# Optimization experiments

Hardware: AMD Instinct MI355X
Metric: run time of the kernel (lower is better)

Reference implementation:

```python
import jax, jax.numpy as jnp
import numpy as np

NHEAD = 8

def layernorm(x, g, b, eps=1e-5):
    mu = x.mean(-1, keepdims=True)
    var = ((x - mu) ** 2).mean(-1, keepdims=True)
    return (x - mu) / jnp.sqrt(var + eps) * g + b

def linear_attention(q, k, v, eps=1e-6):
    # LoFTR kernelized linear attention: phi(x) = elu(x) + 1
    Q = jax.nn.elu(q) + 1.0          # [n, l, h, d]
    K = jax.nn.elu(k) + 1.0          # [n, s, h, d]
    s_len = v.shape[1]
    KV = jnp.einsum("nshd,nshv->nhdv", K, v / s_len)
    Z = 1.0 / (jnp.einsum("nlhd,nhd->nlh", Q, K.sum(axis=1)) + eps)
    return jnp.einsum("nlhd,nhdv,nlh->nlhv", Q, KV, Z) * s_len

def _block(x_base, q, k, v, Wm, W1, W2, g1, b1, g2, b2):
    bs, L, h, dh = q.shape
    msg = linear_attention(q, k, v).reshape(bs, L, h * dh)
    msg = layernorm(msg @ Wm, g1, b1)
    hcat = jnp.concatenate([x_base, msg], axis=2)          # [bs, L, 2*d]
    out = jax.nn.relu(hcat @ W1) @ W2
    return layernorm(out, g2, b2)

def setup_inputs() -> dict:
    key = jax.random.key(0)
    ks = jax.random.split(key, 8)
    bs, L, S, d = 8, 4800, 4800, 256
    w = lambda k, i, o: jax.random.normal(k, (i, o), jnp.float32) * 0.02
    return {
        "x": jax.random.normal(ks[0], (bs, L, d), jnp.float32),
        "source": jax.random.normal(ks[1], (bs, S, d), jnp.float32),
        "Wq": w(ks[2], d, d), "Wk": w(ks[3], d, d), "Wv": w(ks[4], d, d),
        "Wm": w(ks[5], d, d),
        "W1": w(ks[6], 2 * d, 2 * d), "W2": w(ks[7], 2 * d, d),
        "g1": jnp.ones((d,), jnp.float32), "b1": jnp.zeros((d,), jnp.float32),
        "g2": jnp.ones((d,), jnp.float32), "b2": jnp.zeros((d,), jnp.float32),
    }

def reference(x, source, Wq, Wk, Wv, Wm, W1, W2, g1, b1, g2, b2):
    bs, L, d = x.shape
    h = NHEAD
    dh = d // h
    q = (x @ Wq).reshape(bs, L, h, dh)
    k = (source @ Wk).reshape(bs, -1, h, dh)
    v = (source @ Wv).reshape(bs, -1, h, dh)
    # permute-then-view reinterpretations, exactly as in the torch code
    p13 = lambda t: t.transpose(0, 1, 3, 2).reshape(bs, -1, h, dh)  # permute(0,1,3,2)
    p21 = lambda t: t.transpose(0, 2, 1, 3).reshape(bs, -1, h, dh)  # permute(0,2,1,3)
    p32 = lambda t: t.transpose(0, 3, 2, 1).reshape(bs, -1, h, dh)  # permute(0,3,2,1)
    blk = lambda xb, qq, kk, vv: _block(xb, qq, kk, vv, Wm, W1, W2, g1, b1, g2, b2)
    m = blk(x, q, k, v)
    m3 = blk(x, p13(q), p13(k), p13(v))
    x_mid = x + 0.5 * (m + m3)
    m1 = blk(x_mid, p21(q), p21(k), p21(v))
    m2 = blk(x_mid, p32(q), p32(k), p32(v))
    return x_mid + 0.5 * (m1 + m2)
```

## Files before the change

kernel.cpp:

```cpp
#include <hip/hip_runtime.h>
#include <type_traits>
#include <cstdint>
#include <cstddef>

#define L_SEQ 4800
#define DMODEL 256
#define BS 8
#define MROWS (BS*L_SEQ)
#define PERBATCH (L_SEQ*DMODEL)
#define KVSET 67584

typedef __attribute__((ext_vector_type(8))) short bfrag8;
typedef __attribute__((ext_vector_type(4))) float floatx4;

__device__ __forceinline__ float bf2f(unsigned short u){
  union { unsigned int i; float f; } x; x.i = ((unsigned int)u) << 16; return x.f;
}
__device__ __forceinline__ unsigned short f2bf(float f){
  union { float f; unsigned int i; } x; x.f = f;
  x.i += 0x7fff + ((x.i >> 16) & 1);
  return (unsigned short)(x.i >> 16);
}
__device__ __forceinline__ float phi(float x){
  return x > 0.f ? x + 1.f : __expf(x);
}

template<typename TC, bool RELU>
__global__ __launch_bounds__(256) void gemm_mfma(const unsigned short* __restrict__ A,
                                                 const unsigned short* __restrict__ Bt,
                                                 TC* __restrict__ C, int M, int N, int K){
  __shared__ unsigned short Al[128*32];
  __shared__ unsigned short Bl[128*32];
  const int tid  = threadIdx.x;
  const int lane = tid & 63;
  const int wave = tid >> 6;
  const int row0 = blockIdx.y << 7;
  const int col0 = blockIdx.x << 7;
  const int wr0  = (wave & 1) << 6;
  const int wc0  = (wave >> 1) << 6;

  floatx4 acc[4][4] = {};

  const int i0 = tid, i1 = tid + 256;
  const int r0 = i0 >> 2, s0 = i0 & 3;
  const int r1 = i1 >> 2, s1 = i1 & 3;
  const int m = lane & 15, q = lane >> 4;

  for (int k0 = 0; k0 < K; k0 += 32){
    const unsigned short* ga0 = A  + (size_t)(row0 + r0)*K + k0 + s0*8;
    const unsigned short* ga1 = A  + (size_t)(row0 + r1)*K + k0 + s1*8;
    const unsigned short* gb0 = Bt + (size_t)(col0 + r0)*K + k0 + s0*8;
    const unsigned short* gb1 = Bt + (size_t)(col0 + r1)*K + k0 + s1*8;
    __builtin_amdgcn_global_load_lds((const __attribute__((address_space(1))) unsigned int*)ga0,
        (__attribute__((address_space(3))) unsigned int*)(Al + (size_t)i0*8), 16, 0, 0);
    __builtin_amdgcn_global_load_lds((const __attribute__((address_space(1))) unsigned int*)ga1,
        (__attribute__((address_space(3))) unsigned int*)(Al + (size_t)i1*8), 16, 0, 0);
    __builtin_amdgcn_global_load_lds((const __attribute__((address_space(1))) unsigned int*)gb0,
        (__attribute__((address_space(3))) unsigned int*)(Bl + (size_t)i0*8), 16, 0, 0);
    __builtin_amdgcn_global_load_lds((const __attribute__((address_space(1))) unsigned int*)gb1,
        (__attribute__((address_space(3))) unsigned int*)(Bl + (size_t)i1*8), 16, 0, 0);
    __builtin_amdgcn_s_waitcnt(0);
    __syncthreads();

    bfrag8 af[4], bf[4];
    #pragma unroll
    for (int t = 0; t < 4; t++){
      af[t] = *(const bfrag8*)(Al + (size_t)(wr0 + t*16 + m)*32 + q*8);
      bf[t] = *(const bfrag8*)(Bl + (size_t)(wc0 + t*16 + m)*32 + q*8);
    }
    #pragma unroll
    for (int mt = 0; mt < 4; mt++)
      #pragma unroll
      for (int nt = 0; nt < 4; nt++)
        acc[mt][nt] = __builtin_amdgcn_mfma_f32_16x16x32_bf16(af[mt], bf[nt], acc[mt][nt], 0, 0, 0);
    __syncthreads();
  }

  #pragma unroll
  for (int mt = 0; mt < 4; mt++){
    #pragma unroll
    for (int nt = 0; nt < 4; nt++){
      const int col  = col0 + wc0 + nt*16 + m;
      const int rowb = row0 + wr0 + mt*16 + q*4;
      #pragma unroll
      for (int i = 0; i < 4; i++){
        float v = acc[mt][nt][i];
        if (RELU) v = v > 0.f ? v : 0.f;
        if constexpr (std::is_same<TC,float>::value) C[(size_t)(rowb+i)*N + col] = v;
        else                                         C[(size_t)(rowb+i)*N + col] = f2bf(v);
      }
    }
  }
}

__global__ __launch_bounds__(256) void wconv(const float* __restrict__ W, unsigned short* __restrict__ Wt,
                                             int kshift, int N){
  int idx = blockIdx.x*256 + threadIdx.x;
  int kk = idx & ((1 << kshift) - 1);
  int nn = idx >> kshift;
  Wt[idx] = f2bf(W[(size_t)kk*N + nn]);
}
__global__ __launch_bounds__(256) void conv_bf16(const float* __restrict__ in, unsigned short* __restrict__ out){
  int i = blockIdx.x*256 + threadIdx.x;
  float4 v = ((const float4*)in)[i];
  ushort4 o; o.x = f2bf(v.x); o.y = f2bf(v.y); o.z = f2bf(v.z); o.w = f2bf(v.w);
  ((ushort4*)out)[i] = o;
}

__global__ __launch_bounds__(256) void permute1(const unsigned short* __restrict__ sA, unsigned short* __restrict__ dA,
                                                const unsigned short* __restrict__ sB, unsigned short* __restrict__ dB){
  const unsigned short* s = blockIdx.z ? sB : sA;
  unsigned short*       d = blockIdx.z ? dB : dA;
  __shared__ unsigned short tile[1024];
  const int t = threadIdx.x;
  const size_t base = (size_t)blockIdx.x * 1024;
  #pragma unroll
  for (int i = 0; i < 4; i++) tile[i*256 + t] = s[base + i*256 + t];
  __syncthreads();
  const int pg = ((t & 7) << 5) + (t >> 3);
  #pragma unroll
  for (int i = 0; i < 4; i++) d[base + i*256 + t] = tile[i*256 + pg];
}

__global__ __launch_bounds__(256) void permute2(const unsigned short* __restrict__ sA, unsigned short* __restrict__ dA,
                                                const unsigned short* __restrict__ sB, unsigned short* __restrict__ dB){
  const unsigned short* s = blockIdx.z ? sB : sA;
  unsigned short*       d = blockIdx.z ? dB : dA;
  __shared__ unsigned short tile[64*256];
  const int t = threadIdx.x;
  const int rr0 = blockIdx.x * 64;
  const size_t boff = (size_t)blockIdx.y * PERBATCH;
  #pragma unroll
  for (int i = 0; i < 16; i++){
    int u = i*256 + t;
    *(ushort4*)&tile[u*4] = *(const ushort4*)&s[boff + (size_t)rr0*256 + (size_t)u*4];
  }
  __syncthreads();
  #pragma unroll
  for (int i = 0; i < 8; i++){
    #pragma unroll
    for (int w = 0; w < 2; w++){
      int u = w*256 + t;
      int rr = u >> 3, c4 = (u & 7) << 2;
      ushort4 v = *(const ushort4*)&tile[rr*256 + i*32 + c4];
      *(ushort4*)&d[boff + (size_t)i*153600 + (size_t)rr0*32 + (size_t)u*4] = v;
    }
  }
}

__global__ __launch_bounds__(256) void permute3(const unsigned short* __restrict__ sA, unsigned short* __restrict__ dA,
                                                const unsigned short* __restrict__ sB, unsigned short* __restrict__ dB){
  const unsigned short* s = blockIdx.z ? sB : sA;
  unsigned short*       d = blockIdx.z ? dB : dA;
  __shared__ unsigned short tile[64*258];
  const int t = threadIdx.x;
  const int ll0 = blockIdx.x * 64;
  const size_t boff = (size_t)blockIdx.y * PERBATCH;
  #pragma unroll
  for (int i = 0; i < 32; i++){
    int u = i*256 + t;
    int row = u >> 7, col = (u & 127) << 1;
    *(ushort2*)&tile[row*258 + col] = *(const ushort2*)&s[boff + (size_t)(ll0+row)*256 + col];
  }
  __syncthreads();
  const int cw = t >> 6;
  const int ll = t & 63;
  #pragma unroll
  for (int cc = 0; cc < 256; cc += 4){
    int c = cc + cw;
    int sigma = ((c & 31) << 3) + (c >> 5);
    d[boff + (size_t)sigma*4800 + ll0 + ll] = tile[ll*258 + c];
  }
}

__global__ __launch_bounds__(256) void attn_stats(const unsigned short* __restrict__ kq,
                                                  const unsigned short* __restrict__ vq,
                                                  float* __restrict__ KV, float* __restrict__ Ksum){
  const int chunk = blockIdx.x, h = blockIdx.y, n = blockIdx.z;
  const int t = threadIdx.x;
  const int d = t >> 3;
  const int w4 = (t & 7) << 2;
  const size_t boff = (size_t)n * PERBATCH;
  __shared__ float kb[8][32], vb[8][32];
  const int lr = t >> 5, lj = t & 31;
  float a0=0.f, a1=0.f, a2=0.f, a3=0.f, ks=0.f;
  const int s0 = chunk * 240;
  for (int s = s0; s < s0 + 240; s += 8){
    int srci = (s + lr)*256 + (h << 5) + lj;
    kb[lr][lj] = phi(bf2f(kq[boff + srci]));
    vb[lr][lj] = bf2f(vq[boff + srci]);
    __syncthreads();
    #pragma unroll
    for (int r = 0; r < 8; r++){
      float kd = kb[r][d];
      ks += kd;
      a0 += kd * vb[r][w4+0];
      a1 += kd * vb[r][w4+1];
      a2 += kd * vb[r][w4+2];
      a3 += kd * vb[r][w4+3];
    }
    __syncthreads();
  }
  float* kvp = KV + (size_t)((((n<<3)+h)<<5) + d)*32 + w4;
  atomicAdd(kvp+0, a0);
  atomicAdd(kvp+1, a1);
  atomicAdd(kvp+2, a2);
  atomicAdd(kvp+3, a3);
  if ((t & 7) == 0) atomicAdd(Ksum + (((n<<3)+h)<<5) + d, ks);
}

__global__ __launch_bounds__(256) void attn_apply(const unsigned short* __restrict__ qq,
                                                  const float* __restrict__ KV,
                                                  const float* __restrict__ Ksum,
                                                  unsigned short* __restrict__ msg){
  __shared__ float kvs[8192];
  __shared__ float kss[256];
  __shared__ float Qs[4096];
  const int t = threadIdx.x;
  const int n = blockIdx.y;
  const int row0 = blockIdx.x << 4;
  const size_t boff = (size_t)n * PERBATCH;

  #pragma unroll
  for (int i = 0; i < 32; i++) kvs[i*256 + t] = KV[(size_t)n*8192 + i*256 + t];
  kss[t] = Ksum[n*256 + t];
  #pragma unroll
  for (int r = 0; r < 16; r++)
    Qs[r*256 + t] = phi(bf2f(qq[boff + (size_t)(row0 + r)*256 + t]));
  __syncthreads();

  const int h = t >> 5, w = t & 31;
  const float* kvh = kvs + h*1024;
  const float* ksh = kss + h*32;
  float acc[16], den[16];
  #pragma unroll
  for (int r = 0; r < 16; r++){ acc[r] = 0.f; den[r] = 1e-6f; }

  #pragma unroll
  for (int d4 = 0; d4 < 8; d4++){
    const float k0 = kvh[(d4*4+0)*32 + w];
    const float k1 = kvh[(d4*4+1)*32 + w];
    const float k2 = kvh[(d4*4+2)*32 + w];
    const float k3 = kvh[(d4*4+3)*32 + w];
    const float s0 = ksh[d4*4+0], s1 = ksh[d4*4+1], s2 = ksh[d4*4+2], s3 = ksh[d4*4+3];
    #pragma unroll
    for (int r = 0; r < 16; r++){
      float4 qv = *(const float4*)&Qs[r*256 + h*32 + d4*4];
      acc[r] += qv.x*k0 + qv.y*k1 + qv.z*k2 + qv.w*k3;
      den[r] += qv.x*s0 + qv.y*s1 + qv.z*s2 + qv.w*s3;
    }
  }
  #pragma unroll
  for (int r = 0; r < 16; r++)
    msg[boff + (size_t)(row0 + r)*256 + t] = f2bf(acc[r]/den[r]);
}

__device__ __forceinline__ float waveSum(float v){
  #pragma unroll
  for (int o = 32; o > 0; o >>= 1) v += __shfl_xor(v, o, 64);
  return v;
}

__global__ __launch_bounds__(256) void ln_bf16(const float* __restrict__ X, const float* __restrict__ g,
                                               const float* __restrict__ b, unsigned short* __restrict__ dst,
                                               int stride, int off){
  const int lane = threadIdx.x & 63;
  const int row = blockIdx.x*4 + (threadIdx.x >> 6);
  float4 v = ((const float4*)(X + (size_t)row*256))[lane];
  float mu = waveSum(v.x + v.y + v.z + v.w) * (1.f/256.f);
  float x0 = v.x - mu, x1 = v.y - mu, x2 = v.z - mu, x3 = v.w - mu;
  float var = waveSum(x0*x0 + x1*x1 + x2*x2 + x3*x3) * (1.f/256.f);
  float rs = rsqrtf(var + 1e-5f);
  float4 gv = ((const float4*)g)[lane];
  float4 bv = ((const float4*)b)[lane];
  ushort4 o;
  o.x = f2bf(x0*rs*gv.x + bv.x);
  o.y = f2bf(x1*rs*gv.y + bv.y);
  o.z = f2bf(x2*rs*gv.z + bv.z);
  o.w = f2bf(x3*rs*gv.w + bv.w);
  ((ushort4*)(dst + (size_t)row*stride + off))[lane] = o;
}

__global__ __launch_bounds__(256) void ln_acc(const float* __restrict__ X, const float* __restrict__ g,
                                              const float* __restrict__ b, float* __restrict__ macc, int add){
  const int lane = threadIdx.x & 63;
  const int row = blockIdx.x*4 + (threadIdx.x >> 6);
  float4 v = ((const float4*)(X + (size_t)row*256))[lane];
  float mu = waveSum(v.x + v.y + v.z + v.w) * (1.f/256.f);
  float x0 = v.x - mu, x1 = v.y - mu, x2 = v.z - mu, x3 = v.w - mu;
  float var = waveSum(x0*x0 + x1*x1 + x2*x2 + x3*x3) * (1.f/256.f);
  float rs = rsqrtf(var + 1e-5f);
  float4 gv = ((const float4*)g)[lane];
  float4 bv = ((const float4*)b)[lane];
  float4 y;
  y.x = x0*rs*gv.x + bv.x;
  y.y = x1*rs*gv.y + bv.y;
  y.z = x2*rs*gv.z + bv.z;
  y.w = x3*rs*gv.w + bv.w;
  float4* mp = (float4*)(macc + (size_t)row*256) + lane;
  if (add){
    float4 old = *mp;
    y.x += old.x; y.y += old.y; y.z += old.z; y.w += old.w;
  }
  *mp = y;
}

__global__ __launch_bounds__(256) void fill_hcat(const float* __restrict__ x, unsigned short* __restrict__ hcat){
  size_t i = (size_t)blockIdx.x*256 + threadIdx.x;
  hcat[(i >> 8)*512 + (i & 255)] = f2bf(x[i]);
}
__global__ __launch_bounds__(256) void xmid_k(const float* __restrict__ x, const float* __restrict__ macc,
                                              float* __restrict__ xmid, unsigned short* __restrict__ hcat){
  size_t i = (size_t)blockIdx.x*256 + threadIdx.x;
  float v = x[i] + 0.5f*macc[i];
  xmid[i] = v;
  hcat[(i >> 8)*512 + (i & 255)] = f2bf(v);
}
__global__ __launch_bounds__(256) void final_k(float* __restrict__ out, const float* __restrict__ macc){
  size_t i = (size_t)blockIdx.x*256 + threadIdx.x;
  out[i] = out[i] + 0.5f*macc[i];
}
__global__ __launch_bounds__(256) void zero_k(float* __restrict__ p, int n){
  int i = blockIdx.x*256 + threadIdx.x;
  if (i < n) p[i] = 0.f;
}

extern "C" void kernel_launch(void* const* d_in, const int* in_sizes, int n_in,
                              void* d_out, int out_size, void* d_ws, size_t ws_size,
                              hipStream_t stream){
  const float* x   = (const float*)d_in[0];
  const float* src = (const float*)d_in[1];
  const float* Wq  = (const float*)d_in[2];
  const float* Wk  = (const float*)d_in[3];
  const float* Wv  = (const float*)d_in[4];
  const float* Wm  = (const float*)d_in[5];
  const float* W1  = (const float*)d_in[6];
  const float* W2  = (const float*)d_in[7];
  const float* g1  = (const float*)d_in[8];
  const float* b1  = (const float*)d_in[9];
  const float* g2  = (const float*)d_in[10];
  const float* b2  = (const float*)d_in[11];
  float* out = (float*)d_out;

  char* ws = (char*)d_ws;
  size_t off = 0;
  auto alloc = [&](size_t bytes) -> void* {
    void* p = ws + off;
    off += (bytes + 255) & ~(size_t)255;
    return p;
  };
  unsigned short* qB    = (unsigned short*)alloc((size_t)MROWS*256*2);
  unsigned short* kB    = (unsigned short*)alloc((size_t)MROWS*256*2);
  unsigned short* vB    = (unsigned short*)alloc((size_t)MROWS*256*2);
  unsigned short* hcatB = (unsigned short*)alloc((size_t)MROWS*512*2);
  float* t1   = (float*)alloc((size_t)MROWS*256*4);
  float* macc = (float*)alloc((size_t)MROWS*256*4);
  float* KV4  = (float*)alloc((size_t)4*KVSET*4);
  unsigned short* WqT = (unsigned short*)alloc((size_t)256*256*2);
  unsigned short* WkT = (unsigned short*)alloc((size_t)256*256*2);
  unsigned short* WvT = (unsigned short*)alloc((size_t)256*256*2);
  unsigned short* WmT = (unsigned short*)alloc((size_t)256*256*2);
  unsigned short* W1T = (unsigned short*)alloc((size_t)512*512*2);
  unsigned short* W2T = (unsigned short*)alloc((size_t)256*512*2);
  (void)ws_size; (void)in_sizes; (void)n_in; (void)out_size;

  unsigned short* msgB  = kB;
  unsigned short* hidB  = kB;
  unsigned short* srcbf = (unsigned short*)t1;
  unsigned short* xbf   = srcbf + (size_t)MROWS*256;
  unsigned short* qP    = (unsigned short*)t1;
  unsigned short* kP    = (unsigned short*)macc;
  unsigned short* vP    = kP + (size_t)MROWS*256;
  float* xmid = out;

  const dim3 blk(256);

  wconv<<<dim3(256),  blk, 0, stream>>>(Wq, WqT, 8, 256);
  wconv<<<dim3(256),  blk, 0, stream>>>(Wk, WkT, 8, 256);
  wconv<<<dim3(256),  blk, 0, stream>>>(Wv, WvT, 8, 256);
  wconv<<<dim3(256),  blk, 0, stream>>>(Wm, WmT, 8, 256);
  wconv<<<dim3(1024), blk, 0, stream>>>(W1, W1T, 9, 512);
  wconv<<<dim3(512),  blk, 0, stream>>>(W2, W2T, 9, 256);
  conv_bf16<<<dim3(9600), blk, 0, stream>>>(src, srcbf);
  conv_bf16<<<dim3(9600), blk, 0, stream>>>(x,   xbf);

  gemm_mfma<unsigned short, false><<<dim3(2,300), blk, 0, stream>>>(xbf,   WqT, qB, MROWS, 256, 256);
  gemm_mfma<unsigned short, false><<<dim3(2,300), blk, 0, stream>>>(srcbf, WkT, kB, MROWS, 256, 256);
  gemm_mfma<unsigned short, false><<<dim3(2,300), blk, 0, stream>>>(srcbf, WvT, vB, MROWS, 256, 256);

  zero_k<<<dim3(1056), blk, 0, stream>>>(KV4, 4*KVSET);
  attn_stats<<<dim3(20,8,8), blk, 0, stream>>>(kB, vB, KV4 + 0*KVSET, KV4 + 0*KVSET + 65536);
  permute1<<<dim3(9600,1,2), blk, 0, stream>>>(kB, kP, vB, vP);
  attn_stats<<<dim3(20,8,8), blk, 0, stream>>>(kP, vP, KV4 + 1*KVSET, KV4 + 1*KVSET + 65536);
  permute2<<<dim3(75,8,2),  blk, 0, stream>>>(kB, kP, vB, vP);
  attn_stats<<<dim3(20,8,8), blk, 0, stream>>>(kP, vP, KV4 + 2*KVSET, KV4 + 2*KVSET + 65536);
  permute3<<<dim3(75,8,2),  blk, 0, stream>>>(kB, kP, vB, vP);
  attn_stats<<<dim3(20,8,8), blk, 0, stream>>>(kP, vP, KV4 + 3*KVSET, KV4 + 3*KVSET + 65536);

  fill_hcat<<<dim3(MROWS), blk, 0, stream>>>(x, hcatB);

  auto run_block = [&](int mode, int add){
    const float* KV   = KV4 + (size_t)mode*KVSET;
    const float* Ksum = KV + 65536;
    const unsigned short* qsrc = qB;
    if (mode == 1){ permute1<<<dim3(9600,1,1), blk, 0, stream>>>(qB, qP, nullptr, nullptr); qsrc = qP; }
    else if (mode == 2){ permute2<<<dim3(75,8,1), blk, 0, stream>>>(qB, qP, nullptr, nullptr); qsrc = qP; }
    else if (mode == 3){ permute3<<<dim3(75,8,1), blk, 0, stream>>>(qB, qP, nullptr, nullptr); qsrc = qP; }
    attn_apply<<<dim3(300,BS), blk, 0, stream>>>(qsrc, KV, Ksum, msgB);
    gemm_mfma<float, false><<<dim3(2,300), blk, 0, stream>>>(msgB, WmT, t1, MROWS, 256, 256);
    ln_bf16<<<dim3(9600), blk, 0, stream>>>(t1, g1, b1, hcatB, 512, 256);
    gemm_mfma<unsigned short, true><<<dim3(4,300), blk, 0, stream>>>(hcatB, W1T, hidB, MROWS, 512, 512);
    gemm_mfma<float, false><<<dim3(2,300), blk, 0, stream>>>(hidB, W2T, t1, MROWS, 256, 512);
    ln_acc<<<dim3(9600), blk, 0, stream>>>(t1, g2, b2, macc, add);
  };

  run_block(0, 0);
  run_block(1, 1);
  xmid_k<<<dim3(MROWS), blk, 0, stream>>>(x, macc, xmid, hcatB);
  run_block(2, 0);
  run_block(3, 1);
  final_k<<<dim3(MROWS), blk, 0, stream>>>(out, macc);
}
```

Baseline: 998.8 us.

## Fuse attention apply with Wm GEMM+LN, and FFN GEMMs with final LN

Replaces the six-kernel per-block chain (attn_apply, Wm GEMM, LN, W1 GEMM, W2 GEMM, LN-accumulate) with two fused kernels. attn_fused computes the linear-attention message for 64 rows into swizzled LDS, multiplies by Wm with MFMA, applies layernorm and writes bf16 into hcat. ffn_fused keeps the ReLU hidden tile in LDS between the W1 and W2 GEMMs using double-buffered global-to-LDS staging, then applies layernorm and accumulates into macc. This removes the fp32 intermediate round trips through global memory and several launches, at the cost of heavy LDS use (about 138KB per block in the FFN) and lower occupancy.

```diff
diff --git a/kernel.cpp b/kernel.cpp
--- a/kernel.cpp
+++ b/kernel.cpp
@@ -23,6 +23,10 @@
 }
 __device__ __forceinline__ float phi(float x){
   return x > 0.f ? x + 1.f : __expf(x);
+}
+__device__ __forceinline__ void gll16(const void* g, void* l){
+  __builtin_amdgcn_global_load_lds((const __attribute__((address_space(1))) unsigned int*)g,
+      (__attribute__((address_space(3))) unsigned int*)l, 16, 0, 0);
 }
 
 template<typename TC, bool RELU>
@@ -51,14 +55,10 @@
     const unsigned short* ga1 = A  + (size_t)(row0 + r1)*K + k0 + s1*8;
     const unsigned short* gb0 = Bt + (size_t)(col0 + r0)*K + k0 + s0*8;
     const unsigned short* gb1 = Bt + (size_t)(col0 + r1)*K + k0 + s1*8;
-    __builtin_amdgcn_global_load_lds((const __attribute__((address_space(1))) unsigned int*)ga0,
-        (__attribute__((address_space(3))) unsigned int*)(Al + (size_t)i0*8), 16, 0, 0);
-    __builtin_amdgcn_global_load_lds((const __attribute__((address_space(1))) unsigned int*)ga1,
-        (__attribute__((address_space(3))) unsigned int*)(Al + (size_t)i1*8), 16, 0, 0);
-    __builtin_amdgcn_global_load_lds((const __attribute__((address_space(1))) unsigned int*)gb0,
-        (__attribute__((address_space(3))) unsigned int*)(Bl + (size_t)i0*8), 16, 0, 0);
-    __builtin_amdgcn_global_load_lds((const __attribute__((address_space(1))) unsigned int*)gb1,
-        (__attribute__((address_space(3))) unsigned int*)(Bl + (size_t)i1*8), 16, 0, 0);
+    gll16(ga0, Al + (size_t)i0*8);
+    gll16(ga1, Al + (size_t)i1*8);
+    gll16(gb0, Bl + (size_t)i0*8);
+    gll16(gb1, Bl + (size_t)i1*8);
     __builtin_amdgcn_s_waitcnt(0);
     __syncthreads();
 
@@ -209,100 +209,291 @@
   if ((t & 7) == 0) atomicAdd(Ksum + (((n<<3)+h)<<5) + d, ks);
 }
 
-__global__ __launch_bounds__(256) void attn_apply(const unsigned short* __restrict__ qq,
+__global__ __launch_bounds__(256) void attn_fused(const unsigned short* __restrict__ qq,
                                                   const float* __restrict__ KV,
                                                   const float* __restrict__ Ksum,
-                                                  unsigned short* __restrict__ msg){
+                                                  const unsigned short* __restrict__ WmT,
+                                                  const float* __restrict__ g1,
+                                                  const float* __restrict__ b1,
+                                                  unsigned short* __restrict__ hcat){
   __shared__ float kvs[8192];
-  __shared__ float kss[256];
-  __shared__ float Qs[4096];
+  __shared__ char  msgL[32768];
+  __shared__ char  pool[16384];
   const int t = threadIdx.x;
   const int n = blockIdx.y;
-  const int row0 = blockIdx.x << 4;
+  const int row0 = blockIdx.x << 6;
   const size_t boff = (size_t)n * PERBATCH;
 
   #pragma unroll
   for (int i = 0; i < 32; i++) kvs[i*256 + t] = KV[(size_t)n*8192 + i*256 + t];
-  kss[t] = Ksum[n*256 + t];
-  #pragma unroll
-  for (int r = 0; r < 16; r++)
-    Qs[r*256 + t] = phi(bf2f(qq[boff + (size_t)(row0 + r)*256 + t]));
-  __syncthreads();
+  const float kssv = Ksum[n*256 + t];
 
   const int h = t >> 5, w = t & 31;
   const float* kvh = kvs + h*1024;
-  const float* ksh = kss + h*32;
-  float acc[16], den[16];
-  #pragma unroll
-  for (int r = 0; r < 16; r++){ acc[r] = 0.f; den[r] = 1e-6f; }
-
-  #pragma unroll
-  for (int d4 = 0; d4 < 8; d4++){
-    const float k0 = kvh[(d4*4+0)*32 + w];
-    const float k1 = kvh[(d4*4+1)*32 + w];
-    const float k2 = kvh[(d4*4+2)*32 + w];
-    const float k3 = kvh[(d4*4+3)*32 + w];
-    const float s0 = ksh[d4*4+0], s1 = ksh[d4*4+1], s2 = ksh[d4*4+2], s3 = ksh[d4*4+3];
-    #pragma unroll
-    for (int r = 0; r < 16; r++){
-      float4 qv = *(const float4*)&Qs[r*256 + h*32 + d4*4];
-      acc[r] += qv.x*k0 + qv.y*k1 + qv.z*k2 + qv.w*k3;
-      den[r] += qv.x*s0 + qv.y*s1 + qv.z*s2 + qv.w*s3;
-    }
-  }
-  #pragma unroll
-  for (int r = 0; r < 16; r++)
-    msg[boff + (size_t)(row0 + r)*256 + t] = f2bf(acc[r]/den[r]);
-}
-
-__device__ __forceinline__ float waveSum(float v){
-  #pragma unroll
-  for (int o = 32; o > 0; o >>= 1) v += __shfl_xor(v, o, 64);
-  return v;
-}
-
-__global__ __launch_bounds__(256) void ln_bf16(const float* __restrict__ X, const float* __restrict__ g,
-                                               const float* __restrict__ b, unsigned short* __restrict__ dst,
-                                               int stride, int off){
-  const int lane = threadIdx.x & 63;
-  const int row = blockIdx.x*4 + (threadIdx.x >> 6);
-  float4 v = ((const float4*)(X + (size_t)row*256))[lane];
-  float mu = waveSum(v.x + v.y + v.z + v.w) * (1.f/256.f);
-  float x0 = v.x - mu, x1 = v.y - mu, x2 = v.z - mu, x3 = v.w - mu;
-  float var = waveSum(x0*x0 + x1*x1 + x2*x2 + x3*x3) * (1.f/256.f);
-  float rs = rsqrtf(var + 1e-5f);
-  float4 gv = ((const float4*)g)[lane];
-  float4 bv = ((const float4*)b)[lane];
-  ushort4 o;
-  o.x = f2bf(x0*rs*gv.x + bv.x);
-  o.y = f2bf(x1*rs*gv.y + bv.y);
-  o.z = f2bf(x2*rs*gv.z + bv.z);
-  o.w = f2bf(x3*rs*gv.w + bv.w);
-  ((ushort4*)(dst + (size_t)row*stride + off))[lane] = o;
-}
-
-__global__ __launch_bounds__(256) void ln_acc(const float* __restrict__ X, const float* __restrict__ g,
-                                              const float* __restrict__ b, float* __restrict__ macc, int add){
-  const int lane = threadIdx.x & 63;
-  const int row = blockIdx.x*4 + (threadIdx.x >> 6);
-  float4 v = ((const float4*)(X + (size_t)row*256))[lane];
-  float mu = waveSum(v.x + v.y + v.z + v.w) * (1.f/256.f);
-  float x0 = v.x - mu, x1 = v.y - mu, x2 = v.z - mu, x3 = v.w - mu;
-  float var = waveSum(x0*x0 + x1*x1 + x2*x2 + x3*x3) * (1.f/256.f);
-  float rs = rsqrtf(var + 1e-5f);
-  float4 gv = ((const float4*)g)[lane];
-  float4 bv = ((const float4*)b)[lane];
-  float4 y;
-  y.x = x0*rs*gv.x + bv.x;
-  y.y = x1*rs*gv.y + bv.y;
-  y.z = x2*rs*gv.z + bv.z;
-  y.w = x3*rs*gv.w + bv.w;
-  float4* mp = (float4*)(macc + (size_t)row*256) + lane;
-  if (add){
-    float4 old = *mp;
-    y.x += old.x; y.y += old.y; y.z += old.z; y.w += old.w;
-  }
-  *mp = y;
+  float* Qs = (float*)pool;
+
+  for (int p = 0; p < 8; p++){
+    #pragma unroll
+    for (int r = 0; r < 8; r++)
+      Qs[r*256 + t] = phi(bf2f(qq[boff + (size_t)(row0 + p*8 + r)*256 + t]));
+    __syncthreads();
+
+    float acc[8], den[8];
+    #pragma unroll
+    for (int r = 0; r < 8; r++){
+      float dd = Qs[r*256 + t] * kssv;
+      #pragma unroll
+      for (int o = 1; o < 32; o <<= 1) dd += __shfl_xor(dd, o, 64);
+      den[r] = dd + 1e-6f;
+      acc[r] = 0.f;
+    }
+    #pragma unroll
+    for (int d4 = 0; d4 < 8; d4++){
+      const float k0v = kvh[(d4*4+0)*32 + w];
+      const float k1v = kvh[(d4*4+1)*32 + w];
+      const float k2v = kvh[(d4*4+2)*32 + w];
+      const float k3v = kvh[(d4*4+3)*32 + w];
+      #pragma unroll
+      for (int r = 0; r < 8; r++){
+        float4 qv = *(const float4*)&Qs[r*256 + h*32 + d4*4];
+        acc[r] += qv.x*k0v + qv.y*k1v + qv.z*k2v + qv.w*k3v;
+      }
+    }
+    #pragma unroll
+    for (int r = 0; r < 8; r++){
+      int lrow = p*8 + r;
+      int byte = (lrow << 9) + (t << 1);
+      byte ^= (lrow & 7) << 4;
+      *(unsigned short*)(msgL + byte) = f2bf(acc[r] / den[r]);
+    }
+    __syncthreads();
+  }
+
+  const int wave = t >> 6, lane = t & 63, m = lane & 15, qd = lane >> 4;
+  float gv[16], bv[16];
+  #pragma unroll
+  for (int nt = 0; nt < 16; nt++){ gv[nt] = g1[nt*16 + m]; bv[nt] = b1[nt*16 + m]; }
+
+  floatx4 acc[16] = {};
+  for (int ks = 0; ks < 8; ks++){
+    const int k0 = ks << 5;
+    #pragma unroll
+    for (int i = 0; i < 4; i++){
+      int u = (i << 8) + t;
+      int c = u >> 2, q4 = u & 3;
+      gll16(WmT + (size_t)c*256 + k0 + ((q4 ^ (c & 3)) << 3), pool + (u << 4));
+    }
+    asm volatile("s_waitcnt vmcnt(0)" ::: "memory");
+    __builtin_amdgcn_s_barrier();
+    asm volatile("" ::: "memory");
+    const int arow = (wave << 4) + m;
+    int abyte = (arow << 9) + (ks << 6) + (qd << 4);
+    abyte ^= (m & 7) << 4;
+    bfrag8 af = *(const bfrag8*)(msgL + abyte);
+    #pragma unroll
+    for (int nt = 0; nt < 16; nt++){
+      int col = (nt << 4) + m;
+      bfrag8 bf = *(const bfrag8*)(pool + col*64 + ((qd ^ (m & 3)) << 4));
+      acc[nt] = __builtin_amdgcn_mfma_f32_16x16x32_bf16(af, bf, acc[nt], 0, 0, 0);
+    }
+    asm volatile("" ::: "memory");
+    __builtin_amdgcn_s_barrier();
+    asm volatile("" ::: "memory");
+  }
+
+  float mu[4], rs[4];
+  #pragma unroll
+  for (int i = 0; i < 4; i++){
+    float s = 0.f, q = 0.f;
+    #pragma unroll
+    for (int nt = 0; nt < 16; nt++){ float v = acc[nt][i]; s += v; q += v*v; }
+    #pragma unroll
+    for (int o = 1; o < 16; o <<= 1){ s += __shfl_xor(s, o, 64); q += __shfl_xor(q, o, 64); }
+    float mean = s * (1.f/256.f);
+    float var  = q * (1.f/256.f) - mean*mean;
+    mu[i] = mean; rs[i] = rsqrtf(var + 1e-5f);
+  }
+  #pragma unroll
+  for (int nt = 0; nt < 16; nt++){
+    #pragma unroll
+    for (int i = 0; i < 4; i++){
+      int row = (wave << 4) + (qd << 2) + i;
+      int col = (nt << 4) + m;
+      int byte = (row << 9) + (col << 1);
+      byte ^= (row & 7) << 4;
+      *(unsigned short*)(msgL + byte) = f2bf((acc[nt][i] - mu[i]) * rs[i] * gv[nt] + bv[nt]);
+    }
+  }
+  __syncthreads();
+  const size_t gbase = (size_t)(n*4800 + row0) * 512;
+  #pragma unroll
+  for (int i = 0; i < 16; i++){
+    int u = (i << 8) + t;
+    int row = u >> 6, j = u & 63;
+    int byte = ((row << 9) + (j << 3)) ^ ((row & 7) << 4);
+    *(ushort4*)(hcat + gbase + (size_t)row*512 + 256 + (j << 2)) = *(const ushort4*)(msgL + byte);
+  }
+}
+
+__global__ __launch_bounds__(512) void ffn_fused(const unsigned short* __restrict__ hcat,
+                                                 const unsigned short* __restrict__ W1T,
+                                                 const unsigned short* __restrict__ W2T,
+                                                 const float* __restrict__ g2,
+                                                 const float* __restrict__ b2,
+                                                 float* __restrict__ macc, int add){
+  __shared__ char stg[73728];
+  __shared__ char hidm[65536];
+  const int tid = threadIdx.x;
+  const int wave = tid >> 6, lane = tid & 63;
+  const int rg = wave >> 1, ch = wave & 1;
+  const int m = lane & 15, qd = lane >> 4;
+  const int row0 = blockIdx.x << 6;
+
+  float gv[8], bv[8];
+  #pragma unroll
+  for (int nt = 0; nt < 8; nt++){
+    int col = (ch << 7) + nt*16 + m;
+    gv[nt] = g2[col]; bv[nt] = b2[col];
+  }
+
+  auto stage1 = [&](int ks, int b){
+    const int k0 = ks << 5;
+    {
+      int u = tid & 255;
+      int r = u >> 2, q4 = u & 3;
+      gll16(hcat + (size_t)(row0 + r)*512 + k0 + ((q4 ^ (r & 3)) << 3),
+            stg + (b << 12) + (u << 4));
+    }
+    #pragma unroll
+    for (int i = 0; i < 4; i++){
+      int u = (i << 9) + tid;
+      int c = u >> 2, q4 = u & 3;
+      gll16(W1T + (size_t)c*512 + k0 + ((q4 ^ (c & 3)) << 3),
+            stg + 8192 + (b << 15) + (u << 4));
+    }
+  };
+
+  floatx4 acc1[16] = {};
+  stage1(0, 0);
+  asm volatile("s_waitcnt vmcnt(0)" ::: "memory");
+  __builtin_amdgcn_s_barrier();
+  asm volatile("" ::: "memory");
+  for (int ks = 0; ks < 16; ks++){
+    if (ks < 15) stage1(ks+1, (ks+1) & 1);
+    const char* hb = stg + ((ks & 1) << 12);
+    const char* wb = stg + 8192 + ((ks & 1) << 15);
+    const int arow = (rg << 4) + m;
+    bfrag8 af = *(const bfrag8*)(hb + arow*64 + ((qd ^ (m & 3)) << 4));
+    #pragma unroll
+    for (int nt = 0; nt < 16; nt++){
+      int col = (ch << 8) + (nt << 4) + m;
+      bfrag8 bf = *(const bfrag8*)(wb + col*64 + ((qd ^ (m & 3)) << 4));
+      acc1[nt] = __builtin_amdgcn_mfma_f32_16x16x32_bf16(af, bf, acc1[nt], 0, 0, 0);
+    }
+    asm volatile("" ::: "memory");
+    if (ks < 15) asm volatile("s_waitcnt vmcnt(0)" ::: "memory");
+    __builtin_amdgcn_s_barrier();
+    asm volatile("" ::: "memory");
+  }
+
+  #pragma unroll
+  for (int nt = 0; nt < 16; nt++){
+    #pragma unroll
+    for (int i = 0; i < 4; i++){
+      float v = acc1[nt][i];
+      v = v > 0.f ? v : 0.f;
+      int row = (rg << 4) + (qd << 2) + i;
+      int col = (ch << 8) + (nt << 4) + m;
+      int byte = (row << 10) + (col << 1);
+      byte ^= (row & 7) << 4;
+      *(unsigned short*)(hidm + byte) = f2bf(v);
+    }
+  }
+
+  auto stage2 = [&](int ks, int b){
+    const int k0 = ks << 5;
+    #pragma unroll
+    for (int i = 0; i < 2; i++){
+      int u = (i << 9) + tid;
+      int c = u >> 2, q4 = u & 3;
+      gll16(W2T + (size_t)c*512 + k0 + ((q4 ^ (c & 3)) << 3),
+            stg + (b << 14) + (u << 4));
+    }
+  };
+  stage2(0, 0);
+  asm volatile("s_waitcnt vmcnt(0) lgkmcnt(0)" ::: "memory");
+  __builtin_amdgcn_s_barrier();
+  asm volatile("" ::: "memory");
+
+  floatx4 acc2[8] = {};
+  for (int ks = 0; ks < 16; ks++){
+    if (ks < 15) stage2(ks+1, (ks+1) & 1);
+    const char* wb = stg + ((ks & 1) << 14);
+    const int arow = (rg << 4) + m;
+    int abyte = (arow << 10) + (ks << 6) + (qd << 4);
+    abyte ^= (m & 7) << 4;
+    bfrag8 af = *(const bfrag8*)(hidm + abyte);
+    #pragma unroll
+    for (int nt = 0; nt < 8; nt++){
+      int col = (ch << 7) + (nt << 4) + m;
+      bfrag8 bf = *(const bfrag8*)(wb + col*64 + ((qd ^ (m & 3)) << 4));
+      acc2[nt] = __builtin_amdgcn_mfma_f32_16x16x32_bf16(af, bf, acc2[nt], 0, 0, 0);
+    }
+    asm volatile("" ::: "memory");
+    if (ks < 15) asm volatile("s_waitcnt vmcnt(0)" ::: "memory");
+    __builtin_amdgcn_s_barrier();
+    asm volatile("" ::: "memory");
+  }
+
+  float2* LNp = (float2*)(stg + 32768);
+  #pragma unroll
+  for (int i = 0; i < 4; i++){
+    float s = 0.f, q = 0.f;
+    #pragma unroll
+    for (int nt = 0; nt < 8; nt++){ float v = acc2[nt][i]; s += v; q += v*v; }
+    #pragma unroll
+    for (int o = 1; o < 16; o <<= 1){ s += __shfl_xor(s, o, 64); q += __shfl_xor(q, o, 64); }
+    if (m == 0){
+      int row = (rg << 4) + (qd << 2) + i;
+      LNp[row*2 + ch] = make_float2(s, q);
+    }
+  }
+  asm volatile("s_waitcnt lgkmcnt(0)" ::: "memory");
+  __builtin_amdgcn_s_barrier();
+  asm volatile("" ::: "memory");
+
+  float mu[4], rs[4];
+  #pragma unroll
+  for (int i = 0; i < 4; i++){
+    int row = (rg << 4) + (qd << 2) + i;
+    float2 a = LNp[row*2], c = LNp[row*2 + 1];
+    float S = a.x + c.x, Q = a.y + c.y;
+    float mean = S * (1.f/256.f);
+    float var  = Q * (1.f/256.f) - mean*mean;
+    mu[i] = mean; rs[i] = rsqrtf(var + 1e-5f);
+  }
+  float* ysh = (float*)hidm;
+  #pragma unroll
+  for (int nt = 0; nt < 8; nt++){
+    #pragma unroll
+    for (int i = 0; i < 4; i++){
+      int row = (rg << 4) + (qd << 2) + i;
+      int col = (ch << 7) + (nt << 4) + m;
+      ysh[(row << 8) + col] = (acc2[nt][i] - mu[i]) * rs[i] * gv[nt] + bv[nt];
+    }
+  }
+  asm volatile("s_waitcnt lgkmcnt(0)" ::: "memory");
+  __builtin_amdgcn_s_barrier();
+  asm volatile("" ::: "memory");
+  #pragma unroll
+  for (int i = 0; i < 8; i++){
+    int u = (i << 9) + tid;
+    int row = u >> 6, c4 = u & 63;
+    float4 v = *(const float4*)(ysh + (row << 8) + (c4 << 2));
+    float4* gp = (float4*)(macc + (size_t)(row0 + row)*256) + c4;
+    if (add){ float4 o = *gp; v.x += o.x; v.y += o.y; v.z += o.z; v.w += o.w; }
+    *gp = v;
+  }
 }
 
 __global__ __launch_bounds__(256) void fill_hcat(const float* __restrict__ x, unsigned short* __restrict__ hcat){
@@ -364,8 +555,6 @@
   unsigned short* W2T = (unsigned short*)alloc((size_t)256*512*2);
   (void)ws_size; (void)in_sizes; (void)n_in; (void)out_size;
 
-  unsigned short* msgB  = kB;
-  unsigned short* hidB  = kB;
   unsigned short* srcbf = (unsigned short*)t1;
   unsigned short* xbf   = srcbf + (size_t)MROWS*256;
   unsigned short* qP    = (unsigned short*)t1;
@@ -406,12 +595,8 @@
     if (mode == 1){ permute1<<<dim3(9600,1,1), blk, 0, stream>>>(qB, qP, nullptr, nullptr); qsrc = qP; }
     else if (mode == 2){ permute2<<<dim3(75,8,1), blk, 0, stream>>>(qB, qP, nullptr, nullptr); qsrc = qP; }
     else if (mode == 3){ permute3<<<dim3(75,8,1), blk, 0, stream>>>(qB, qP, nullptr, nullptr); qsrc = qP; }
-    attn_apply<<<dim3(300,BS), blk, 0, stream>>>(qsrc, KV, Ksum, msgB);
-    gemm_mfma<float, false><<<dim3(2,300), blk, 0, stream>>>(msgB, WmT, t1, MROWS, 256, 256);
-    ln_bf16<<<dim3(9600), blk, 0, stream>>>(t1, g1, b1, hcatB, 512, 256);
-    gemm_mfma<unsigned short, true><<<dim3(4,300), blk, 0, stream>>>(hcatB, W1T, hidB, MROWS, 512, 512);
-    gemm_mfma<float, false><<<dim3(2,300), blk, 0, stream>>>(hidB, W2T, t1, MROWS, 256, 512);
-    ln_acc<<<dim3(9600), blk, 0, stream>>>(t1, g2, b2, macc, add);
+    attn_fused<<<dim3(75,BS), blk, 0, stream>>>(qsrc, KV, Ksum, WmT, g1, b1, hcatB);
+    ffn_fused<<<dim3(600), dim3(512), 0, stream>>>(hcatB, W1T, W2T, g2, b2, macc, add);
   };
 
   run_block(0, 0);
```

Measured after the change: 1.108 ms. 1.11x slower.
